# Optimization experiments

Hardware: AMD Instinct MI355X
Metric: run time of the kernel (lower is better)

## Reference

```python
import jax, jax.numpy as jnp
import numpy as np
from jax import lax

SIGMAS = [0.5, 1.0, 2.0]
CHANNELS = 64

def _gaussian_kernel(sigma, channels):
    k = int(6 * sigma + 1) | 1
    x = np.arange(k, dtype=np.float32) - k // 2
    k1 = np.exp(-x ** 2 / (2 * sigma ** 2))
    k2 = np.outer(k1, k1)
    k2 = k2 / k2.sum()
    # depthwise weight layout OIHW with feature_group_count=channels: (C, 1, k, k)
    w = np.broadcast_to(k2[None, None], (channels, 1, k, k)).copy()
    return jnp.asarray(w)

_KERNELS = [_gaussian_kernel(s, CHANNELS) for s in SIGMAS]

def setup_inputs() -> dict:
    key = jax.random.key(0)
    k1, k2, k3 = jax.random.split(key, 3)
    x = jax.random.normal(k1, (8, CHANNELS, 256, 256), dtype=jnp.float32)
    fusion_w = jax.random.normal(k2, (CHANNELS, CHANNELS * len(SIGMAS)), dtype=jnp.float32) * 0.05
    fusion_b = jax.random.normal(k3, (CHANNELS,), dtype=jnp.float32) * 0.05
    return {"x": x, "fusion_w": fusion_w, "fusion_b": fusion_b}

def _depthwise(x, w):
    return lax.conv_general_dilated(
        x, w, window_strides=(1, 1), padding="SAME",
        dimension_numbers=("NCHW", "OIHW", "NCHW"),
        feature_group_count=x.shape[1])

def reference(x, fusion_w, fusion_b):
    # multi-scale depthwise Gaussian blurs, concat on channel dim
    multi_scale = jnp.concatenate([_depthwise(x, w) for w in _KERNELS], axis=1)  # [B, 3C, H, W]
    # 1x1 fusion conv + bias
    fused = jnp.einsum("bchw,oc->bohw", multi_scale, fusion_w) + fusion_b[None, :, None, None]
    return x + fused
```

## Files before the change

### kernel.cpp

```cpp
#include <hip/hip_runtime.h>
#include <hip/hip_bf16.h>
#include <math.h>

#define B_  8
#define C_  64
#define H_  256
#define W_  256
#define HW_ (H_*W_)
#define J_  192
#define TH_ 32

typedef __attribute__((ext_vector_type(8))) short short8;
typedef __attribute__((ext_vector_type(4))) float f32x4;

__device__ __forceinline__ ushort f2bf(float f) {
    union { float f; uint u; } v; v.f = f;
    uint u = v.u;
    return (ushort)((u + 0x7fffu + ((u >> 16) & 1u)) >> 16);
}
__device__ __forceinline__ float bf2f(ushort s) {
    union { uint u; float f; } v; v.u = ((uint)s) << 16;
    return v.f;
}
__device__ __forceinline__ uint pk(float a, float b) {
    return (uint)f2bf(a) | ((uint)f2bf(b) << 16);
}
__device__ __forceinline__ float bflo(uint u) {
    union { uint u; float f; } v; v.u = u << 16; return v.f;
}
__device__ __forceinline__ float bfhi(uint u) {
    union { uint u; float f; } v; v.u = u & 0xffff0000u; return v.f;
}

__global__ __launch_bounds__(256) void k1_mix(
    const float* __restrict__ x, const float* __restrict__ fw,
    ushort* __restrict__ v)
{
    __shared__ ushort lxs[256 * 64];

    const int b      = blockIdx.x >> 8;
    const int pxbase = (blockIdx.x & 255) << 8;
    const int t      = threadIdx.x;
    const int lane   = t & 63;
    const int wv_    = t >> 6;

    {
        const int cg = lane;
        const float* xb = x + (size_t)b * C_ * HW_ + pxbase + 4 * cg;
#pragma unroll
        for (int i = 0; i < 4; ++i) {
            const int cb = wv_ * 4 + i * 16;
            const int c4 = wv_ + i * 4;
            float4 r0 = *(const float4*)(xb + (size_t)(cb + 0) * HW_);
            float4 r1 = *(const float4*)(xb + (size_t)(cb + 1) * HW_);
            float4 r2 = *(const float4*)(xb + (size_t)(cb + 2) * HW_);
            float4 r3 = *(const float4*)(xb + (size_t)(cb + 3) * HW_);
            const int sbase = c4 ^ (cg & 15);
            ushort* dst = &lxs[(4 * cg) * 64];
            *(uint2*)(dst + 0*64 + ((sbase ^ 0) * 4)) = make_uint2(pk(r0.x, r1.x), pk(r2.x, r3.x));
            *(uint2*)(dst + 1*64 + ((sbase ^ 4) * 4)) = make_uint2(pk(r0.y, r1.y), pk(r2.y, r3.y));
            *(uint2*)(dst + 2*64 + ((sbase ^ 8) * 4)) = make_uint2(pk(r0.z, r1.z), pk(r2.z, r3.z));
            *(uint2*)(dst + 3*64 + ((sbase ^ 12) * 4)) = make_uint2(pk(r0.w, r1.w), pk(r2.w, r3.w));
        }
    }

    const int n = lane & 15;
    const int q = lane >> 4;
    union Frag { short8 v; uint u[4]; };
    Frag wf[3][2];
#pragma unroll
    for (int i = 0; i < 3; ++i) {
        const int j  = (wv_ * 3 + i) * 16 + n;
        const float* wr = fw + (size_t)(j & 63) * J_ + (j >> 6) * 64;
#pragma unroll
        for (int kh = 0; kh < 2; ++kh) {
            float4 w0 = *(const float4*)(wr + kh * 32 + q * 8);
            float4 w1 = *(const float4*)(wr + kh * 32 + q * 8 + 4);
            wf[i][kh].u[0] = pk(w0.x, w0.y);
            wf[i][kh].u[1] = pk(w0.z, w0.w);
            wf[i][kh].u[2] = pk(w1.x, w1.y);
            wf[i][kh].u[3] = pk(w1.z, w1.w);
        }
    }

    __syncthreads();

    for (int mt = 0; mt < 16; ++mt) {
        const int px = mt * 16 + (lane & 15);
        const ushort* row = &lxs[px * 64];
        const int s = ((px >> 2) & 15) ^ ((px & 3) << 2);
        Frag a0, a1;
        {
            uint2 lo  = *(const uint2*)&row[((2*q    ) ^ s) * 4];
            uint2 hi  = *(const uint2*)&row[((2*q + 1) ^ s) * 4];
            a0.u[0] = lo.x;  a0.u[1] = lo.y;  a0.u[2] = hi.x;  a0.u[3] = hi.y;
            uint2 lo1 = *(const uint2*)&row[((8 + 2*q    ) ^ s) * 4];
            uint2 hi1 = *(const uint2*)&row[((8 + 2*q + 1) ^ s) * 4];
            a1.u[0] = lo1.x; a1.u[1] = lo1.y; a1.u[2] = hi1.x; a1.u[3] = hi1.y;
        }
#pragma unroll
        for (int i = 0; i < 3; ++i) {
            f32x4 acc = {0.f, 0.f, 0.f, 0.f};
            acc = __builtin_amdgcn_mfma_f32_16x16x32_bf16(a0.v, wf[i][0].v, acc, 0, 0, 0);
            acc = __builtin_amdgcn_mfma_f32_16x16x32_bf16(a1.v, wf[i][1].v, acc, 0, 0, 0);
            const int j   = (wv_ * 3 + i) * 16 + n;
            const int pxg = pxbase + mt * 16 + q * 4;
            *(uint2*)&v[(size_t)(b * J_ + j) * HW_ + pxg] =
                make_uint2(pk(acc[0], acc[1]), pk(acc[2], acc[3]));
        }
    }
}

struct Taps {
    float g0[5];
    float g1[7];
    float g2[13];
};

template<int R, int G>
__device__ __forceinline__ void blur_scale(
    const ushort* __restrict__ vplane, const float* __restrict__ g,
    int row0, int cg, float4* acc)
{
    const int NG  = 2 * G + 1;
    const int OFF = 4 * G - R;
    const int K   = 2 * R + 1;
#pragma unroll
    for (int k = 0; k < 8 + 2 * R; ++k) {
        const int gh = row0 - R + k;
        if (gh >= 0 && gh < H_) {
            const ushort* vr = vplane + (size_t)gh * W_;
            float win[NG * 4];
#pragma unroll
            for (int gi = 0; gi < NG; ++gi) {
                const int gg = cg - G + gi;
                uint2 d = (gg >= 0 && gg < 64) ? *(const uint2*)(vr + gg * 4)
                                               : make_uint2(0u, 0u);
                win[gi*4+0] = bflo(d.x); win[gi*4+1] = bfhi(d.x);
                win[gi*4+2] = bflo(d.y); win[gi*4+3] = bfhi(d.y);
            }
            float t0 = 0.f, t1 = 0.f, t2 = 0.f, t3 = 0.f;
#pragma unroll
            for (int dd = 0; dd < K; ++dd) {
                const float gd = g[dd];
                t0 += gd * win[OFF + dd + 0];
                t1 += gd * win[OFF + dd + 1];
                t2 += gd * win[OFF + dd + 2];
                t3 += gd * win[OFF + dd + 3];
            }
            const int ilo = (k - 2 * R) > 0 ? (k - 2 * R) : 0;
            const int ihi = k < 7 ? k : 7;
#pragma unroll
            for (int i = ilo; i <= ihi; ++i) {
                const float gd = g[k - i];
                acc[i].x += gd * t0;
                acc[i].y += gd * t1;
                acc[i].z += gd * t2;
                acc[i].w += gd * t3;
            }
        }
    }
}

__global__ __launch_bounds__(256, 4) void k2_blur(
    const ushort* __restrict__ v, const float* __restrict__ x,
    const float* __restrict__ bias, float* __restrict__ out,
    Taps taps)
{
    const int t    = blockIdx.x;
    const int tile = t & 7;
    const int o    = (t >> 3) & 63;
    const int b    = t >> 9;
    const int cg   = threadIdx.x & 63;
    const int rw   = threadIdx.x >> 6;
    const int c0   = cg * 4;
    const int row0 = tile * TH_ + rw * 8;

    float4 acc[8];
#pragma unroll
    for (int i = 0; i < 8; ++i) acc[i] = make_float4(0.f, 0.f, 0.f, 0.f);

    const ushort* vp = v + (size_t)(b * J_ + o) * HW_;
    blur_scale<2, 1>(vp,                        taps.g0, row0, cg, acc);
    blur_scale<3, 1>(vp + (size_t)C_ * HW_,     taps.g1, row0, cg, acc);
    blur_scale<6, 2>(vp + (size_t)(2*C_) * HW_, taps.g2, row0, cg, acc);

    const float* xp = x   + ((size_t)b * C_ + o) * HW_ + (size_t)row0 * W_;
    float*       op = out + ((size_t)b * C_ + o) * HW_ + (size_t)row0 * W_;
    const float bo = bias[o];
#pragma unroll
    for (int i = 0; i < 8; ++i) {
        float4 xv = *(const float4*)&xp[(size_t)i * W_ + c0];
        float4 r;
        r.x = xv.x + bo + acc[i].x;
        r.y = xv.y + bo + acc[i].y;
        r.z = xv.z + bo + acc[i].z;
        r.w = xv.w + bo + acc[i].w;
        *(float4*)&op[(size_t)i * W_ + c0] = r;
    }
}

static void make_taps(Taps& t)
{
    auto fill = [](float* g, int k, double sigma) {
        int r = k / 2;
        double s = 0.0;
        for (int i = 0; i < k; ++i) {
            double w = exp(-(double)((i - r) * (i - r)) / (2.0 * sigma * sigma));
            g[i] = (float)w;
            s += w;
        }
        for (int i = 0; i < k; ++i) g[i] = (float)((double)g[i] / s);
    };
    fill(t.g0, 5, 0.5);
    fill(t.g1, 7, 1.0);
    fill(t.g2, 13, 2.0);
}

extern "C" void kernel_launch(void* const* d_in, const int* in_sizes, int n_in,
                              void* d_out, int out_size, void* d_ws, size_t ws_size,
                              hipStream_t stream)
{
    const float* x  = (const float*)d_in[0];
    const float* fw = (const float*)d_in[1];
    const float* fb = (const float*)d_in[2];
    float* out = (float*)d_out;
    ushort* v = (ushort*)d_ws;

    Taps taps;
    make_taps(taps);

    k1_mix<<<dim3(B_ * (HW_ / 256)), dim3(256), 0, stream>>>(x, fw, v);
    k2_blur<<<dim3(B_ * C_ * (H_ / TH_)), dim3(256), 0, stream>>>(v, x, fb, out, taps);
}
```

Measured before the change: 431.0 us.

## Split separable blur into LDS-staged horizontal pass and vertical pass with smaller tiles

```diff
diff --git a/kernel.cpp b/kernel.cpp
--- a/kernel.cpp
+++ b/kernel.cpp
@@ -8,7 +8,6 @@
 #define W_  256
 #define HW_ (H_*W_)
 #define J_  192
-#define TH_ 32
 
 typedef __attribute__((ext_vector_type(8))) short short8;
 typedef __attribute__((ext_vector_type(4))) float f32x4;
@@ -111,6 +110,9 @@
     }
 }
 
+#define TH2_ 16
+#define TROWS_ (TH2_+4 + TH2_+6 + TH2_+12)
+
 struct Taps {
     float g0[5];
     float g1[7];
@@ -118,46 +120,56 @@
 };
 
 template<int R, int G>
-__device__ __forceinline__ void blur_scale(
+__device__ __forceinline__ void hjob(
     const ushort* __restrict__ vplane, const float* __restrict__ g,
-    int row0, int cg, float4* acc)
+    ushort* __restrict__ dstrow, int gh, int cg)
 {
     const int NG  = 2 * G + 1;
     const int OFF = 4 * G - R;
     const int K   = 2 * R + 1;
-#pragma unroll
-    for (int k = 0; k < 8 + 2 * R; ++k) {
-        const int gh = row0 - R + k;
-        if (gh >= 0 && gh < H_) {
-            const ushort* vr = vplane + (size_t)gh * W_;
-            float win[NG * 4];
-#pragma unroll
-            for (int gi = 0; gi < NG; ++gi) {
-                const int gg = cg - G + gi;
-                uint2 d = (gg >= 0 && gg < 64) ? *(const uint2*)(vr + gg * 4)
-                                               : make_uint2(0u, 0u);
-                win[gi*4+0] = bflo(d.x); win[gi*4+1] = bfhi(d.x);
-                win[gi*4+2] = bflo(d.y); win[gi*4+3] = bfhi(d.y);
-            }
-            float t0 = 0.f, t1 = 0.f, t2 = 0.f, t3 = 0.f;
-#pragma unroll
-            for (int dd = 0; dd < K; ++dd) {
-                const float gd = g[dd];
-                t0 += gd * win[OFF + dd + 0];
-                t1 += gd * win[OFF + dd + 1];
-                t2 += gd * win[OFF + dd + 2];
-                t3 += gd * win[OFF + dd + 3];
-            }
-            const int ilo = (k - 2 * R) > 0 ? (k - 2 * R) : 0;
-            const int ihi = k < 7 ? k : 7;
-#pragma unroll
-            for (int i = ilo; i <= ihi; ++i) {
-                const float gd = g[k - i];
-                acc[i].x += gd * t0;
-                acc[i].y += gd * t1;
-                acc[i].z += gd * t2;
-                acc[i].w += gd * t3;
-            }
+    float o0 = 0.f, o1 = 0.f, o2 = 0.f, o3 = 0.f;
+    if (gh >= 0 && gh < H_) {
+        const ushort* vr = vplane + (size_t)gh * W_;
+        float win[NG * 4];
+#pragma unroll
+        for (int gi = 0; gi < NG; ++gi) {
+            const int gg = cg - G + gi;
+            uint2 d = (gg >= 0 && gg < 64) ? *(const uint2*)(vr + gg * 4)
+                                           : make_uint2(0u, 0u);
+            win[gi*4+0] = bflo(d.x); win[gi*4+1] = bfhi(d.x);
+            win[gi*4+2] = bflo(d.y); win[gi*4+3] = bfhi(d.y);
+        }
+#pragma unroll
+        for (int dd = 0; dd < K; ++dd) {
+            const float gd = g[dd];
+            o0 += gd * win[OFF + dd + 0];
+            o1 += gd * win[OFF + dd + 1];
+            o2 += gd * win[OFF + dd + 2];
+            o3 += gd * win[OFF + dd + 3];
+        }
+    }
+    *(uint2*)&dstrow[4 * cg] = make_uint2(pk(o0, o1), pk(o2, o3));
+}
+
+template<int R>
+__device__ __forceinline__ void vjob(
+    const ushort* __restrict__ tmp0, const float* __restrict__ g,
+    int cg, float4* acc)
+{
+#pragma unroll
+    for (int k = 0; k < 4 + 2 * R; ++k) {
+        uint2 raw = *(const uint2*)&tmp0[k * W_ + 4 * cg];
+        const float f0 = bflo(raw.x), f1 = bfhi(raw.x);
+        const float f2 = bflo(raw.y), f3 = bfhi(raw.y);
+        const int ilo = (k - 2 * R) > 0 ? (k - 2 * R) : 0;
+        const int ihi = k < 3 ? k : 3;
+#pragma unroll
+        for (int i = ilo; i <= ihi; ++i) {
+            const float gd = g[k - i];
+            acc[i].x += gd * f0;
+            acc[i].y += gd * f1;
+            acc[i].z += gd * f2;
+            acc[i].w += gd * f3;
         }
     }
 }
@@ -167,29 +179,42 @@
     const float* __restrict__ bias, float* __restrict__ out,
     Taps taps)
 {
+    __shared__ ushort tmp[TROWS_ * W_];
+
     const int t    = blockIdx.x;
-    const int tile = t & 7;
-    const int o    = (t >> 3) & 63;
-    const int b    = t >> 9;
+    const int tile = t & 15;
+    const int o    = (t >> 4) & 63;
+    const int b    = t >> 10;
+    const int h0   = tile * TH2_;
     const int cg   = threadIdx.x & 63;
     const int rw   = threadIdx.x >> 6;
     const int c0   = cg * 4;
-    const int row0 = tile * TH_ + rw * 8;
-
-    float4 acc[8];
-#pragma unroll
-    for (int i = 0; i < 8; ++i) acc[i] = make_float4(0.f, 0.f, 0.f, 0.f);
 
     const ushort* vp = v + (size_t)(b * J_ + o) * HW_;
-    blur_scale<2, 1>(vp,                        taps.g0, row0, cg, acc);
-    blur_scale<3, 1>(vp + (size_t)C_ * HW_,     taps.g1, row0, cg, acc);
-    blur_scale<6, 2>(vp + (size_t)(2*C_) * HW_, taps.g2, row0, cg, acc);
-
+
+    for (int r = rw; r < TH2_ + 4; r += 4)
+        hjob<2, 1>(vp,                        taps.g0, &tmp[r * W_],            h0 - 2 + r, cg);
+    for (int r = rw; r < TH2_ + 6; r += 4)
+        hjob<3, 1>(vp + (size_t)C_ * HW_,     taps.g1, &tmp[(20 + r) * W_],     h0 - 3 + r, cg);
+    for (int r = rw; r < TH2_ + 12; r += 4)
+        hjob<6, 2>(vp + (size_t)(2*C_) * HW_, taps.g2, &tmp[(42 + r) * W_],     h0 - 6 + r, cg);
+
+    __syncthreads();
+
+    float4 acc[4];
+#pragma unroll
+    for (int i = 0; i < 4; ++i) acc[i] = make_float4(0.f, 0.f, 0.f, 0.f);
+
+    vjob<2>(&tmp[(0  + rw * 4) * W_], taps.g0, cg, acc);
+    vjob<3>(&tmp[(20 + rw * 4) * W_], taps.g1, cg, acc);
+    vjob<6>(&tmp[(42 + rw * 4) * W_], taps.g2, cg, acc);
+
+    const int row0 = h0 + rw * 4;
     const float* xp = x   + ((size_t)b * C_ + o) * HW_ + (size_t)row0 * W_;
     float*       op = out + ((size_t)b * C_ + o) * HW_ + (size_t)row0 * W_;
     const float bo = bias[o];
 #pragma unroll
-    for (int i = 0; i < 8; ++i) {
+    for (int i = 0; i < 4; ++i) {
         float4 xv = *(const float4*)&xp[(size_t)i * W_ + c0];
         float4 r;
         r.x = xv.x + bo + acc[i].x;
@@ -231,5 +256,5 @@
     make_taps(taps);
 
     k1_mix<<<dim3(B_ * (HW_ / 256)), dim3(256), 0, stream>>>(x, fw, v);
-    k2_blur<<<dim3(B_ * C_ * (H_ / TH_)), dim3(256), 0, stream>>>(v, x, fb, out, taps);
-}
+    k2_blur<<<dim3(B_ * C_ * (H_ / TH2_)), dim3(256), 0, stream>>>(v, x, fb, out, taps);
+}
```

Result: no change. 432.4 us (+0.3%).
